# Optimization experiments

Measured on AMD Instinct MI355X. Metric: run time of the kernel, lower is better.

Reference implementation:

```python
import jax, jax.numpy as jnp
import numpy as np

N = 100000  # nodes

def gcn_layer(x, W, b, src, dst, norm):
    # x: [N, Fin] -> [N, Fout]; symmetric-normalized aggregation (PyG GCNConv)
    h = x @ W                                   # linear first (no bias yet)
    msg = h[src] * norm[:, None]                # gather + edge-wise scale
    out = jax.ops.segment_sum(msg, dst, num_segments=N)  # scatter-add to targets
    return out + b

def _prep_edges(edge_index):
    # add self loops
    loops = jnp.arange(N, dtype=edge_index.dtype)
    src = jnp.concatenate([edge_index[0], loops])
    dst = jnp.concatenate([edge_index[1], loops])
    # deg computed on target nodes with unit edge weights
    deg = jax.ops.segment_sum(jnp.ones_like(dst, dtype=jnp.float32), dst, num_segments=N)
    dinv = jnp.where(deg > 0, jax.lax.rsqrt(deg), 0.0)
    norm = dinv[src] * dinv[dst]
    return src, dst, norm

def setup_inputs() -> dict:
    key = jax.random.key(0)
    ks = jax.random.split(key, 8)
    F_in, H1, H2, C = 512, 256, 64, 10
    E = 3200000
    x = jax.random.normal(ks[0], (N, F_in), dtype=jnp.float32)
    edge_index = jax.random.randint(ks[1], (2, E), 0, N, dtype=jnp.int64)
    def glorot(k, fan_in, fan_out):
        s = jnp.sqrt(6.0 / (fan_in + fan_out))
        return jax.random.uniform(k, (fan_in, fan_out), jnp.float32, -s, s)
    return {
        "x": x,
        "edge_index": edge_index,
        "W1": glorot(ks[2], F_in, H1), "b1": jnp.zeros((H1,), jnp.float32),
        "W2": glorot(ks[3], H1, H2),   "b2": jnp.zeros((H2,), jnp.float32),
        "W3": glorot(ks[4], H2, C),    "b3": jnp.zeros((C,), jnp.float32),
    }

def reference(x, edge_index, W1, b1, W2, b2, W3, b3):
    src, dst, norm = _prep_edges(edge_index)
    h = jax.nn.relu(gcn_layer(x, W1, b1, src, dst, norm))
    h = jax.nn.relu(gcn_layer(h, W2, b2, src, dst, norm))
    h = gcn_layer(h, W3, b3, src, dst, norm)
    return jax.nn.log_softmax(h, axis=1)
```

## Files before the change

kernel.cpp:

```cpp
#include <hip/hip_runtime.h>
#include <math.h>

#define NNODES 100000
#define NEDGES 3200000
#define NB 391
#define PB 512
#define CHUNK 6250

typedef __attribute__((ext_vector_type(4))) float f32x4;
typedef __attribute__((ext_vector_type(2))) float f32x2;
typedef __attribute__((ext_vector_type(8))) short bf16x8;

__device__ __forceinline__ float bf2f(ushort u) {
    union { unsigned u; float f; } v; v.u = ((unsigned)u) << 16; return v.f;
}
__device__ __forceinline__ ushort f2bf(float f) {
    union { float f; unsigned u; } v; v.f = f;
    unsigned r = v.u + 0x7FFFu + ((v.u >> 16) & 1u);
    return (ushort)(r >> 16);
}

__device__ __forceinline__ unsigned pack_bf2(float f0, float f1) {
    union { float f; unsigned u; } a, b; a.f = f0; b.f = f1;
#if __has_builtin(__builtin_amdgcn_perm)
    return __builtin_amdgcn_perm(b.u, a.u, 0x07060302u);
#else
    return (b.u & 0xFFFF0000u) | (a.u >> 16);
#endif
}

#if __has_builtin(__builtin_amdgcn_cvt_pk_fp8_f32) && __has_builtin(__builtin_amdgcn_cvt_pk_f32_fp8)
#define FP8_HW 1
#else
#define FP8_HW 0
#endif

__device__ __forceinline__ unsigned fp8enc_sw(float f) {
    union { float f; unsigned u; } v; v.f = f;
    unsigned sign = v.u >> 31;
    float a = fabsf(f);
    if (a >= 448.0f) return (sign << 7) | 0x7E;
    if (a < 0.0009765625f) return sign << 7;
    unsigned u = v.u & 0x7FFFFFFFu;
    u += 0x7FFFFu + ((u >> 20) & 1u);
    int e2 = (int)(u >> 23) - 127;
    if (e2 < -6) {
        int m = (int)(a * 512.0f + 0.5f); if (m > 7) m = 7;
        return (sign << 7) | (unsigned)m;
    }
    if (e2 > 8) return (sign << 7) | 0x7E;
    unsigned mant = (u >> 20) & 7u;
    return (sign << 7) | ((unsigned)(e2 + 7) << 3) | mant;
}
__device__ __forceinline__ float fp8dec_sw(unsigned b) {
    unsigned s = b >> 7, e = (b >> 3) & 0xF, m = b & 7;
    float v;
    if (e == 0) v = (float)m * 0.001953125f;
    else { union { unsigned u; float f; } x; x.u = ((e + 120u) << 23) | (m << 20); v = x.f; }
    return s ? -v : v;
}

__device__ __forceinline__ unsigned char f2fp8(float f) {
#if FP8_HW
    return (unsigned char)(__builtin_amdgcn_cvt_pk_fp8_f32(f, 0.f, 0, false) & 0xFF);
#else
    return (unsigned char)fp8enc_sw(f);
#endif
}
__device__ __forceinline__ void fp8x4_acc(unsigned w, float& ax, float& ay, float& az, float& aw) {
#if FP8_HW
    f32x2 lo = __builtin_amdgcn_cvt_pk_f32_fp8((int)w, false);
    f32x2 hi = __builtin_amdgcn_cvt_pk_f32_fp8((int)w, true);
    ax += lo[0]; ay += lo[1]; az += hi[0]; aw += hi[1];
#else
    ax += fp8dec_sw(w & 0xFF); ay += fp8dec_sw((w >> 8) & 0xFF);
    az += fp8dec_sw((w >> 16) & 0xFF); aw += fp8dec_sw(w >> 24);
#endif
}

__global__ void bucket_hist(const int* __restrict__ dst, int e, int* __restrict__ hist) {
    __shared__ int h[NB];
    const int b = blockIdx.x, t = threadIdx.x;
    for (int j = t; j < NB; j += 256) h[j] = 0;
    __syncthreads();
    const int lo = b * CHUNK;
    int hi = lo + CHUNK; if (hi > e) hi = e;
    for (int i = lo + t; i < hi; i += 256)
        atomicAdd(&h[dst[i] >> 8], 1);
    __syncthreads();
    for (int j = t; j < NB; j += 256) hist[b * NB + j] = h[j];
}

__global__ void scan_buckets(int* __restrict__ hist, int* __restrict__ btotal) {
    __shared__ int s[256];
    const int j = blockIdx.x, t = threadIdx.x;
    int v0 = hist[(2 * t) * NB + j];
    int v1 = hist[(2 * t + 1) * NB + j];
    int p = v0 + v1;
    s[t] = p;
    __syncthreads();
    for (int off = 1; off < 256; off <<= 1) {
        int u = (t >= off) ? s[t - off] : 0;
        __syncthreads();
        s[t] += u;
        __syncthreads();
    }
    int excl = s[t] - p;
    hist[(2 * t) * NB + j] = excl;
    hist[(2 * t + 1) * NB + j] = excl + v0;
    if (t == 255) btotal[j] = s[255];
}

__global__ void scan_btotal(const int* __restrict__ btotal, int* __restrict__ bstart, int e) {
    __shared__ int s[512];
    const int t = threadIdx.x;
    int v = (t < NB) ? btotal[t] : 0;
    s[t] = v;
    __syncthreads();
    for (int off = 1; off < 512; off <<= 1) {
        int u = (t >= off) ? s[t - off] : 0;
        __syncthreads();
        s[t] += u;
        __syncthreads();
    }
    if (t < NB) bstart[t] = s[t] - v;
    if (t == 0) bstart[NB] = e;
}

__global__ void bucket_scatter(const int* __restrict__ src, const int* __restrict__ dst, int e,
                               const int* __restrict__ hist, const int* __restrict__ bstart,
                               unsigned* __restrict__ bucketed) {
    __shared__ int off[NB];
    const int b = blockIdx.x, t = threadIdx.x;
    for (int j = t; j < NB; j += 256) off[j] = bstart[j] + hist[b * NB + j];
    __syncthreads();
    const int lo = b * CHUNK;
    int hi = lo + CHUNK; if (hi > e) hi = e;
    for (int i = lo + t; i < hi; i += 256) {
        int d = dst[i];
        int j = d >> 8;
        int p = atomicAdd(&off[j], 1);
        bucketed[p] = (unsigned)src[i] | ((unsigned)(d & 255) << 24);
    }
}

__global__ void bucket_finalize(const unsigned* __restrict__ bucketed, const int* __restrict__ bstart,
                                float* __restrict__ dinv, int* __restrict__ rowptr,
                                int* __restrict__ esrc, int n, int e) {
    __shared__ int h[256];
    __shared__ int s[256];
    __shared__ int rp[256];
    const int j = blockIdx.x, t = threadIdx.x;
    h[t] = 0;
    __syncthreads();
    const int lo = bstart[j], hi = bstart[j + 1];
    for (int i = lo + t; i < hi; i += 256)
        atomicAdd(&h[bucketed[i] >> 24], 1);
    __syncthreads();
    const int c = h[t] + 1;
    s[t] = c;
    __syncthreads();
    for (int off = 1; off < 256; off <<= 1) {
        int u = (t >= off) ? s[t - off] : 0;
        __syncthreads();
        s[t] += u;
        __syncthreads();
    }
    const int excl = s[t] - c;
    const int base = j << 8;
    const int node = base + t;
    const int myrp = bstart[j] + base + excl;
    rp[t] = myrp;
    if (node < n) {
        dinv[node] = rsqrtf((float)c);
        rowptr[node] = myrp;
        esrc[myrp] = node;
    }
    if (j == 0 && t == 0) rowptr[n] = e + n;
    h[t] = 0;
    __syncthreads();
    for (int i = lo + t; i < hi; i += 256) {
        unsigned ed = bucketed[i];
        int l = ed >> 24;
        int off = atomicAdd(&h[l], 1);
        esrc[rp[l] + 1 + off] = (int)(ed & 0xFFFFFFu);
    }
}

__global__ void conv_wt(const float* __restrict__ W, ushort* __restrict__ Wt,
                        int K, int N, int Npad) {
    int idx = blockIdx.x * blockDim.x + threadIdx.x;
    if (idx >= Npad * K) return;
    int n = idx / K, k = idx % K;
    Wt[idx] = (n < N) ? f2bf(W[(size_t)k * N + n]) : (ushort)0;
}

template <int BM, int BN, int BK, int WM, int WN>
__launch_bounds__(WM* WN * 64)
__global__ void gemm_f32a(const float* __restrict__ A, const ushort* __restrict__ Bt,
                          const float* __restrict__ dinv, unsigned char* __restrict__ Cout,
                          int M, int N, int K) {
    constexpr int NT = WM * WN * 64;
    __shared__ __align__(16) float Asf[BM][BK];
    __shared__ __align__(16) ushort Bs[BN][BK];
    const int tid = threadIdx.x;
    const int wid = tid >> 6, lane = tid & 63;
    const int wr = wid / WN, wc = wid % WN;
    constexpr int TM = BM / WM, TN = BN / WN;
    constexpr int FM = TM / 16, FN = TN / 16;
    const int m0 = blockIdx.y * BM, n0 = blockIdx.x * BN;
    const int ln = lane & 15, ks4 = (lane >> 4) * 2;

    f32x4 acc[FM][FN] = {};

    constexpr int CPRA = BK / 4;
    constexpr int ACH = BM * CPRA;
    constexpr int CPRB = BK / 8;
    constexpr int BCH = BN * CPRB;

    for (int k0 = 0; k0 < K; k0 += BK) {
        #pragma unroll
        for (int it = 0; it < ACH / NT; ++it) {
            int c = it * NT + tid;
            int row = c >> 3, chs = c & 7;
            int gch = chs ^ (row & 7);
            int gm = m0 + row; if (gm >= M) gm = M - 1;
            const float* gp = &A[(size_t)gm * K + k0 + gch * 4];
            __builtin_amdgcn_global_load_lds(
                (const __attribute__((address_space(1))) void*)gp,
                (__attribute__((address_space(3))) void*)((char*)&Asf[0][0] + c * 16),
                16, 0, 0);
        }
        #pragma unroll
        for (int it = 0; it < BCH / NT; ++it) {
            int c = it * NT + tid;
            int row = c / CPRB, ch = c % CPRB;
            const ushort* gp = &Bt[(size_t)(n0 + row) * K + k0 + ch * 8];
            __builtin_amdgcn_global_load_lds(
                (const __attribute__((address_space(1))) void*)gp,
                (__attribute__((address_space(3))) void*)((char*)&Bs[0][0] + c * 16),
                16, 0, 0);
        }
        __syncthreads();

        bf16x8 af[FM], bfr[FN];
        #pragma unroll
        for (int mi = 0; mi < FM; ++mi) {
            int r = wr * TM + mi * 16 + ln;
            const char* rowp = (const char*)&Asf[0][0] + r * (BK * 4);
            float4 a0 = *(const float4*)(rowp + ((ks4 ^ (r & 7)) * 16));
            float4 a1 = *(const float4*)(rowp + (((ks4 + 1) ^ (r & 7)) * 16));
            union { unsigned w[4]; bf16x8 v; } u;
            u.w[0] = pack_bf2(a0.x, a0.y);
            u.w[1] = pack_bf2(a0.z, a0.w);
            u.w[2] = pack_bf2(a1.x, a1.y);
            u.w[3] = pack_bf2(a1.z, a1.w);
            af[mi] = u.v;
        }
        const int ks = (lane >> 4) * 8;
        #pragma unroll
        for (int nj = 0; nj < FN; ++nj)
            bfr[nj] = *(const bf16x8*)&Bs[wc * TN + nj * 16 + ln][ks];
        #pragma unroll
        for (int mi = 0; mi < FM; ++mi)
            #pragma unroll
            for (int nj = 0; nj < FN; ++nj)
                acc[mi][nj] = __builtin_amdgcn_mfma_f32_16x16x32_bf16(af[mi], bfr[nj], acc[mi][nj], 0, 0, 0);
        __syncthreads();
    }

    const int rbase = (lane >> 4) * 4;
    #pragma unroll
    for (int mi = 0; mi < FM; ++mi) {
        #pragma unroll
        for (int r = 0; r < 4; ++r) {
            int gm = m0 + wr * TM + mi * 16 + rbase + r;
            if (gm >= M) continue;
            float d = dinv[gm];
            #pragma unroll
            for (int nj = 0; nj < FN; ++nj) {
                int gn = n0 + wc * TN + nj * 16 + ln;
                Cout[(size_t)gm * N + gn] = f2fp8(acc[mi][nj][r] * d);
            }
        }
    }
}

template <int BM, int BN, int BK, int WM, int WN, int OUTK>
__launch_bounds__(WM* WN * 64)
__global__ void gemm_bf16(const ushort* __restrict__ A, const ushort* __restrict__ Bt,
                          const float* __restrict__ dinv, void* __restrict__ Cout,
                          int M, int N, int K) {
    constexpr int NT = WM * WN * 64;
    __shared__ __align__(16) ushort As[BM][BK];
    __shared__ __align__(16) ushort Bs[BN][BK];
    const int tid = threadIdx.x;
    const int wid = tid >> 6, lane = tid & 63;
    const int wr = wid / WN, wc = wid % WN;
    constexpr int TM = BM / WM, TN = BN / WN;
    constexpr int FM = TM / 16, FN = TN / 16;
    const int m0 = blockIdx.y * BM, n0 = blockIdx.x * BN;
    const int ln = lane & 15, ks = (lane >> 4) * 8;

    f32x4 acc[FM][FN] = {};

    constexpr int ACH = BM * BK / 8;
    constexpr int BCH = BN * BK / 8;
    constexpr int CPR = BK / 8;

    for (int k0 = 0; k0 < K; k0 += BK) {
        #pragma unroll
        for (int it = 0; it < (ACH + NT - 1) / NT; ++it) {
            int c = it * NT + tid;
            if ((ACH % NT == 0) || (c < ACH)) {
                int row = c / CPR, ch = c % CPR;
                int gm = m0 + row; if (gm >= M) gm = M - 1;
                const ushort* gp = &A[(size_t)gm * K + k0 + ch * 8];
                __builtin_amdgcn_global_load_lds(
                    (const __attribute__((address_space(1))) void*)gp,
                    (__attribute__((address_space(3))) void*)((char*)&As[0][0] + c * 16),
                    16, 0, 0);
            }
        }
        #pragma unroll
        for (int it = 0; it < (BCH + NT - 1) / NT; ++it) {
            int c = it * NT + tid;
            if ((BCH % NT == 0) || (c < BCH)) {
                int row = c / CPR, ch = c % CPR;
                const ushort* gp = &Bt[(size_t)(n0 + row) * K + k0 + ch * 8];
                __builtin_amdgcn_global_load_lds(
                    (const __attribute__((address_space(1))) void*)gp,
                    (__attribute__((address_space(3))) void*)((char*)&Bs[0][0] + c * 16),
                    16, 0, 0);
            }
        }
        __syncthreads();

        bf16x8 af[FM], bfr[FN];
        #pragma unroll
        for (int mi = 0; mi < FM; ++mi)
            af[mi] = *(const bf16x8*)&As[wr * TM + mi * 16 + ln][ks];
        #pragma unroll
        for (int nj = 0; nj < FN; ++nj)
            bfr[nj] = *(const bf16x8*)&Bs[wc * TN + nj * 16 + ln][ks];
        #pragma unroll
        for (int mi = 0; mi < FM; ++mi)
            #pragma unroll
            for (int nj = 0; nj < FN; ++nj)
                acc[mi][nj] = __builtin_amdgcn_mfma_f32_16x16x32_bf16(af[mi], bfr[nj], acc[mi][nj], 0, 0, 0);
        __syncthreads();
    }

    const int rbase = (lane >> 4) * 4;
    #pragma unroll
    for (int mi = 0; mi < FM; ++mi) {
        #pragma unroll
        for (int r = 0; r < 4; ++r) {
            int gm = m0 + wr * TM + mi * 16 + rbase + r;
            if (gm >= M) continue;
            float d = dinv[gm];
            #pragma unroll
            for (int nj = 0; nj < FN; ++nj) {
                int gn = n0 + wc * TN + nj * 16 + ln;
                float v = acc[mi][nj][r] * d;
                if (OUTK == 1)      ((float*)Cout)[(size_t)gm * N + gn] = v;
                else if (OUTK == 0) ((ushort*)Cout)[(size_t)gm * N + gn] = f2bf(v);
                else                ((unsigned char*)Cout)[(size_t)gm * N + gn] = f2fp8(v);
            }
        }
    }
}

__global__ void agg1_fp8(const unsigned* __restrict__ h, const int* __restrict__ rowptr,
                         const int* __restrict__ esrc, const float* __restrict__ dinv,
                         const float* __restrict__ bias, ushort* __restrict__ out, int n) {
    const int wid = threadIdx.x >> 6, lane = threadIdx.x & 63;
    const int i = blockIdx.x * 4 + wid;
    if (i >= n) return;
    const int lo = rowptr[i], hi = rowptr[i + 1];
    float ax = 0.f, ay = 0.f, az = 0.f, aw = 0.f;
    int e = lo;
    for (; e + 7 < hi; e += 8) {
        int s[8];
        unsigned w[8];
        #pragma unroll
        for (int q = 0; q < 8; ++q) s[q] = esrc[e + q];
        #pragma unroll
        for (int q = 0; q < 8; ++q) w[q] = h[(size_t)s[q] * 64 + lane];
        #pragma unroll
        for (int q = 0; q < 8; ++q) fp8x4_acc(w[q], ax, ay, az, aw);
    }
    for (; e < hi; ++e)
        fp8x4_acc(h[(size_t)esrc[e] * 64 + lane], ax, ay, az, aw);

    float d = dinv[i];
    const int f0 = lane * 4;
    float4 b = *(const float4*)&bias[f0];
    ushort4 o;
    o.x = f2bf(fmaxf(ax * d + b.x, 0.f));
    o.y = f2bf(fmaxf(ay * d + b.y, 0.f));
    o.z = f2bf(fmaxf(az * d + b.z, 0.f));
    o.w = f2bf(fmaxf(aw * d + b.w, 0.f));
    *(ushort4*)&out[(size_t)i * 256 + f0] = o;
}

__global__ void agg2_fp8(const unsigned* __restrict__ h, const int* __restrict__ rowptr,
                         const int* __restrict__ esrc, const float* __restrict__ dinv,
                         const float* __restrict__ bias, ushort* __restrict__ out, int n) {
    const int g = threadIdx.x >> 4, j = threadIdx.x & 15;
    const int i = blockIdx.x * 16 + g;
    if (i >= n) return;
    const int lo = rowptr[i], hi = rowptr[i + 1];
    float ax = 0.f, ay = 0.f, az = 0.f, aw = 0.f;
    int e = lo;
    for (; e + 3 < hi; e += 4) {
        int s0 = esrc[e], s1 = esrc[e + 1], s2 = esrc[e + 2], s3 = esrc[e + 3];
        unsigned w0 = h[(size_t)s0 * 16 + j];
        unsigned w1 = h[(size_t)s1 * 16 + j];
        unsigned w2 = h[(size_t)s2 * 16 + j];
        unsigned w3 = h[(size_t)s3 * 16 + j];
        fp8x4_acc(w0, ax, ay, az, aw);
        fp8x4_acc(w1, ax, ay, az, aw);
        fp8x4_acc(w2, ax, ay, az, aw);
        fp8x4_acc(w3, ax, ay, az, aw);
    }
    for (; e < hi; ++e)
        fp8x4_acc(h[(size_t)esrc[e] * 16 + j], ax, ay, az, aw);

    float d = dinv[i];
    const int f0 = j * 4;
    float4 b = *(const float4*)&bias[f0];
    ushort4 o;
    o.x = f2bf(fmaxf(ax * d + b.x, 0.f));
    o.y = f2bf(fmaxf(ay * d + b.y, 0.f));
    o.z = f2bf(fmaxf(az * d + b.z, 0.f));
    o.w = f2bf(fmaxf(aw * d + b.w, 0.f));
    *(ushort4*)&out[(size_t)i * 64 + f0] = o;
}

__global__ void agg3_logsoftmax(const ushort* __restrict__ h3, const int* __restrict__ rowptr,
                                const int* __restrict__ esrc, const float* __restrict__ dinv,
                                const float* __restrict__ bias, float* __restrict__ out, int n) {
    const int g = threadIdx.x >> 3, j = threadIdx.x & 7;
    const int i = blockIdx.x * 32 + g;
    if (i >= n) return;
    const int lo = rowptr[i], hi = rowptr[i + 1];
    float a0 = 0.f, a1 = 0.f;
    int e = lo;
    for (; e + 3 < hi; e += 4) {
        int s0 = esrc[e], s1 = esrc[e + 1], s2 = esrc[e + 2], s3 = esrc[e + 3];
        unsigned w0 = *(const unsigned*)&h3[(size_t)s0 * 16 + 2 * j];
        unsigned w1 = *(const unsigned*)&h3[(size_t)s1 * 16 + 2 * j];
        unsigned w2 = *(const unsigned*)&h3[(size_t)s2 * 16 + 2 * j];
        unsigned w3 = *(const unsigned*)&h3[(size_t)s3 * 16 + 2 * j];
        a0 += bf2f((ushort)(w0 & 0xFFFF)) + bf2f((ushort)(w1 & 0xFFFF))
            + bf2f((ushort)(w2 & 0xFFFF)) + bf2f((ushort)(w3 & 0xFFFF));
        a1 += bf2f((ushort)(w0 >> 16)) + bf2f((ushort)(w1 >> 16))
            + bf2f((ushort)(w2 >> 16)) + bf2f((ushort)(w3 >> 16));
    }
    for (; e < hi; ++e) {
        unsigned w = *(const unsigned*)&h3[(size_t)esrc[e] * 16 + 2 * j];
        a0 += bf2f((ushort)(w & 0xFFFF));
        a1 += bf2f((ushort)(w >> 16));
    }
    const int f0 = 2 * j;
    float d = dinv[i];
    float v0 = (f0 < 10) ? (a0 * d + bias[f0]) : -INFINITY;
    float v1 = (f0 + 1 < 10) ? (a1 * d + bias[f0 + 1]) : -INFINITY;
    float m = fmaxf(v0, v1);
    #pragma unroll
    for (int off = 1; off < 8; off <<= 1) m = fmaxf(m, __shfl_xor(m, off, 8));
    float ex = ((f0 < 10) ? expf(v0 - m) : 0.f) + ((f0 + 1 < 10) ? expf(v1 - m) : 0.f);
    #pragma unroll
    for (int off = 1; off < 8; off <<= 1) ex += __shfl_xor(ex, off, 8);
    float ls = logf(ex);
    if (f0 < 10)     out[(size_t)i * 10 + f0] = v0 - m - ls;
    if (f0 + 1 < 10) out[(size_t)i * 10 + f0 + 1] = v1 - m - ls;
}

extern "C" void kernel_launch(void* const* d_in, const int* in_sizes, int n_in,
                              void* d_out, int out_size, void* d_ws, size_t ws_size,
                              hipStream_t stream) {
    const int N = NNODES, E = NEDGES;
    const float* x  = (const float*)d_in[0];
    const int*   ei = (const int*)d_in[1];
    const float* W1 = (const float*)d_in[2];
    const float* b1 = (const float*)d_in[3];
    const float* W2 = (const float*)d_in[4];
    const float* b2 = (const float*)d_in[5];
    const float* W3 = (const float*)d_in[6];
    const float* b3 = (const float*)d_in[7];
    float* out = (float*)d_out;
    const int* src = ei;
    const int* dst = ei + E;

    char* ws = (char*)d_ws;
    size_t off = 0;
    auto alloc = [&](size_t bytes) -> void* {
        void* p = ws + off;
        off = (off + bytes + 255) & ~(size_t)255;
        return p;
    };
    float* dinv   = (float*)alloc((size_t)N * 4);
    int*   rowptr = (int*)alloc((size_t)(N + 1) * 4);
    int*   btotal = (int*)alloc((size_t)NB * 4);
    int*   bstart = (int*)alloc((size_t)(NB + 1) * 4);
    int*   esrc   = (int*)alloc((size_t)(E + N) * 4);
    ushort* W1t   = (ushort*)alloc((size_t)256 * 512 * 2);
    ushort* W2t   = (ushort*)alloc((size_t)64 * 256 * 2);
    ushort* W3t   = (ushort*)alloc((size_t)16 * 64 * 2);
    ushort* h3b   = (ushort*)alloc((size_t)N * 16 * 2);
    ushort* buf1  = (ushort*)alloc((size_t)N * 256 * 2);
    ushort* buf2  = (ushort*)alloc((size_t)N * 256 * 2);
    int*   hist   = (int*)buf1;
    unsigned* bucketed = (unsigned*)buf2;
    unsigned char* h1fp8 = (unsigned char*)buf1;
    unsigned char* h2fp8 = (unsigned char*)buf1;

    const int T = 256;
    bucket_hist<<<PB, T, 0, stream>>>(dst, E, hist);
    scan_buckets<<<NB, T, 0, stream>>>(hist, btotal);
    scan_btotal<<<1, 512, 0, stream>>>(btotal, bstart, E);
    bucket_scatter<<<PB, T, 0, stream>>>(src, dst, E, hist, bstart, bucketed);
    bucket_finalize<<<NB, T, 0, stream>>>(bucketed, bstart, dinv, rowptr, esrc, N, E);

    conv_wt<<<(256 * 512 + T - 1) / T, T, 0, stream>>>(W1, W1t, 512, 256, 256);
    conv_wt<<<(64 * 256 + T - 1) / T, T, 0, stream>>>(W2, W2t, 256, 64, 64);
    conv_wt<<<(16 * 64 + T - 1) / T, T, 0, stream>>>(W3, W3t, 64, 10, 16);

    const int MB = (N + 127) / 128;

    gemm_f32a<128, 256, 32, 2, 4><<<dim3(1, MB), 512, 0, stream>>>(x, W1t, dinv, h1fp8, N, 256, 512);
    agg1_fp8<<<(N + 3) / 4, 256, 0, stream>>>((const unsigned*)h1fp8, rowptr, esrc, dinv, b1, buf2, N);

    gemm_bf16<128, 64, 32, 2, 2, 2><<<dim3(1, MB), 256, 0, stream>>>(buf2, W2t, dinv, h2fp8, N, 64, 256);
    agg2_fp8<<<(N + 15) / 16, 256, 0, stream>>>((const unsigned*)h2fp8, rowptr, esrc, dinv, b2, buf2, N);

    gemm_bf16<128, 16, 32, 4, 1, 0><<<dim3(1, MB), 256, 0, stream>>>(buf2, W3t, dinv, h3b, N, 16, 64);
    agg3_logsoftmax<<<(N + 31) / 32, 256, 0, stream>>>(h3b, rowptr, esrc, dinv, b3, out, N);
}
```

Baseline: 390.4 us.

## Store layer-1/2 activations and W2/W3 in FP8, use FP8 MFMA GEMMs

The aggregation kernels now write their ReLU outputs as FP8 bytes instead of bf16. The second and third GEMMs read those FP8 activations together with FP8-converted weights through the fp8 MFMA instruction. This halves the bytes written by agg1/agg2 and read by the small GEMMs. Accumulators also use packed f32x2 adds after the fp8 conversion. The trade-off is extra quantization error on activations and weights.

```diff
diff --git a/kernel.cpp b/kernel.cpp
--- a/kernel.cpp
+++ b/kernel.cpp
@@ -67,14 +67,13 @@
     return (unsigned char)fp8enc_sw(f);
 #endif
 }
-__device__ __forceinline__ void fp8x4_acc(unsigned w, float& ax, float& ay, float& az, float& aw) {
+__device__ __forceinline__ void fp8x4_acc2(unsigned w, f32x2& a01, f32x2& a23) {
 #if FP8_HW
-    f32x2 lo = __builtin_amdgcn_cvt_pk_f32_fp8((int)w, false);
-    f32x2 hi = __builtin_amdgcn_cvt_pk_f32_fp8((int)w, true);
-    ax += lo[0]; ay += lo[1]; az += hi[0]; aw += hi[1];
+    a01 += __builtin_amdgcn_cvt_pk_f32_fp8((int)w, false);
+    a23 += __builtin_amdgcn_cvt_pk_f32_fp8((int)w, true);
 #else
-    ax += fp8dec_sw(w & 0xFF); ay += fp8dec_sw((w >> 8) & 0xFF);
-    az += fp8dec_sw((w >> 16) & 0xFF); aw += fp8dec_sw(w >> 24);
+    a01[0] += fp8dec_sw(w & 0xFF); a01[1] += fp8dec_sw((w >> 8) & 0xFF);
+    a23[0] += fp8dec_sw((w >> 16) & 0xFF); a23[1] += fp8dec_sw(w >> 24);
 #endif
 }
 
@@ -193,6 +192,14 @@
     if (idx >= Npad * K) return;
     int n = idx / K, k = idx % K;
     Wt[idx] = (n < N) ? f2bf(W[(size_t)k * N + n]) : (ushort)0;
+}
+
+__global__ void conv_wt8(const float* __restrict__ W, unsigned char* __restrict__ Wt,
+                         int K, int N, int Npad) {
+    int idx = blockIdx.x * blockDim.x + threadIdx.x;
+    if (idx >= Npad * K) return;
+    int n = idx / K, k = idx % K;
+    Wt[idx] = (n < N) ? f2fp8(W[(size_t)k * N + n]) : (unsigned char)0;
 }
 
 template <int BM, int BN, int BK, int WM, int WN>
@@ -288,25 +295,25 @@
 
 template <int BM, int BN, int BK, int WM, int WN, int OUTK>
 __launch_bounds__(WM* WN * 64)
-__global__ void gemm_bf16(const ushort* __restrict__ A, const ushort* __restrict__ Bt,
-                          const float* __restrict__ dinv, void* __restrict__ Cout,
-                          int M, int N, int K) {
+__global__ void gemm_fp8(const unsigned char* __restrict__ A, const unsigned char* __restrict__ Bt,
+                         const float* __restrict__ dinv, void* __restrict__ Cout,
+                         int M, int N, int K) {
     constexpr int NT = WM * WN * 64;
-    __shared__ __align__(16) ushort As[BM][BK];
-    __shared__ __align__(16) ushort Bs[BN][BK];
+    __shared__ __align__(16) unsigned char As[BM][BK];
+    __shared__ __align__(16) unsigned char Bs[BN][BK];
     const int tid = threadIdx.x;
     const int wid = tid >> 6, lane = tid & 63;
     const int wr = wid / WN, wc = wid % WN;
     constexpr int TM = BM / WM, TN = BN / WN;
     constexpr int FM = TM / 16, FN = TN / 16;
     const int m0 = blockIdx.y * BM, n0 = blockIdx.x * BN;
-    const int ln = lane & 15, ks = (lane >> 4) * 8;
+    const int ln = lane & 15;
 
     f32x4 acc[FM][FN] = {};
 
-    constexpr int ACH = BM * BK / 8;
-    constexpr int BCH = BN * BK / 8;
-    constexpr int CPR = BK / 8;
+    constexpr int CPR = BK / 16;
+    constexpr int ACH = BM * CPR;
+    constexpr int BCH = BN * CPR;
 
     for (int k0 = 0; k0 < K; k0 += BK) {
         #pragma unroll
@@ -315,7 +322,7 @@
             if ((ACH % NT == 0) || (c < ACH)) {
                 int row = c / CPR, ch = c % CPR;
                 int gm = m0 + row; if (gm >= M) gm = M - 1;
-                const ushort* gp = &A[(size_t)gm * K + k0 + ch * 8];
+                const unsigned char* gp = &A[(size_t)gm * K + k0 + ch * 16];
                 __builtin_amdgcn_global_load_lds(
                     (const __attribute__((address_space(1))) void*)gp,
                     (__attribute__((address_space(3))) void*)((char*)&As[0][0] + c * 16),
@@ -327,7 +334,7 @@
             int c = it * NT + tid;
             if ((BCH % NT == 0) || (c < BCH)) {
                 int row = c / CPR, ch = c % CPR;
-                const ushort* gp = &Bt[(size_t)(n0 + row) * K + k0 + ch * 8];
+                const unsigned char* gp = &Bt[(size_t)(n0 + row) * K + k0 + ch * 16];
                 __builtin_amdgcn_global_load_lds(
                     (const __attribute__((address_space(1))) void*)gp,
                     (__attribute__((address_space(3))) void*)((char*)&Bs[0][0] + c * 16),
@@ -336,18 +343,18 @@
         }
         __syncthreads();
 
-        bf16x8 af[FM], bfr[FN];
+        long af[FM], bfr[FN];
         #pragma unroll
         for (int mi = 0; mi < FM; ++mi)
-            af[mi] = *(const bf16x8*)&As[wr * TM + mi * 16 + ln][ks];
+            af[mi] = ((const long*)&As[0][0])[(wr * TM + mi * 16 + ln) * (BK / 8) + (lane >> 4)];
         #pragma unroll
         for (int nj = 0; nj < FN; ++nj)
-            bfr[nj] = *(const bf16x8*)&Bs[wc * TN + nj * 16 + ln][ks];
+            bfr[nj] = ((const long*)&Bs[0][0])[(wc * TN + nj * 16 + ln) * (BK / 8) + (lane >> 4)];
         #pragma unroll
         for (int mi = 0; mi < FM; ++mi)
             #pragma unroll
             for (int nj = 0; nj < FN; ++nj)
-                acc[mi][nj] = __builtin_amdgcn_mfma_f32_16x16x32_bf16(af[mi], bfr[nj], acc[mi][nj], 0, 0, 0);
+                acc[mi][nj] = __builtin_amdgcn_mfma_f32_16x16x32_fp8_fp8(af[mi], bfr[nj], acc[mi][nj], 0, 0, 0);
         __syncthreads();
     }
 
@@ -363,9 +370,8 @@
             for (int nj = 0; nj < FN; ++nj) {
                 int gn = n0 + wc * TN + nj * 16 + ln;
                 float v = acc[mi][nj][r] * d;
-                if (OUTK == 1)      ((float*)Cout)[(size_t)gm * N + gn] = v;
-                else if (OUTK == 0) ((ushort*)Cout)[(size_t)gm * N + gn] = f2bf(v);
-                else                ((unsigned char*)Cout)[(size_t)gm * N + gn] = f2fp8(v);
+                if (OUTK == 0) ((ushort*)Cout)[(size_t)gm * N + gn] = f2bf(v);
+                else           ((unsigned char*)Cout)[(size_t)gm * N + gn] = f2fp8(v);
             }
         }
     }
@@ -373,12 +379,12 @@
 
 __global__ void agg1_fp8(const unsigned* __restrict__ h, const int* __restrict__ rowptr,
                          const int* __restrict__ esrc, const float* __restrict__ dinv,
-                         const float* __restrict__ bias, ushort* __restrict__ out, int n) {
+                         const float* __restrict__ bias, unsigned char* __restrict__ out, int n) {
     const int wid = threadIdx.x >> 6, lane = threadIdx.x & 63;
     const int i = blockIdx.x * 4 + wid;
     if (i >= n) return;
     const int lo = rowptr[i], hi = rowptr[i + 1];
-    float ax = 0.f, ay = 0.f, az = 0.f, aw = 0.f;
+    f32x2 a01 = {0.f, 0.f}, a23 = {0.f, 0.f};
     int e = lo;
     for (; e + 7 < hi; e += 8) {
         int s[8];
@@ -388,30 +394,30 @@
         #pragma unroll
         for (int q = 0; q < 8; ++q) w[q] = h[(size_t)s[q] * 64 + lane];
         #pragma unroll
-        for (int q = 0; q < 8; ++q) fp8x4_acc(w[q], ax, ay, az, aw);
+        for (int q = 0; q < 8; ++q) fp8x4_acc2(w[q], a01, a23);
     }
     for (; e < hi; ++e)
-        fp8x4_acc(h[(size_t)esrc[e] * 64 + lane], ax, ay, az, aw);
+        fp8x4_acc2(h[(size_t)esrc[e] * 64 + lane], a01, a23);
 
     float d = dinv[i];
     const int f0 = lane * 4;
     float4 b = *(const float4*)&bias[f0];
-    ushort4 o;
-    o.x = f2bf(fmaxf(ax * d + b.x, 0.f));
-    o.y = f2bf(fmaxf(ay * d + b.y, 0.f));
-    o.z = f2bf(fmaxf(az * d + b.z, 0.f));
-    o.w = f2bf(fmaxf(aw * d + b.w, 0.f));
-    *(ushort4*)&out[(size_t)i * 256 + f0] = o;
+    uchar4 o;
+    o.x = f2fp8(fmaxf(a01[0] * d + b.x, 0.f));
+    o.y = f2fp8(fmaxf(a01[1] * d + b.y, 0.f));
+    o.z = f2fp8(fmaxf(a23[0] * d + b.z, 0.f));
+    o.w = f2fp8(fmaxf(a23[1] * d + b.w, 0.f));
+    *(uchar4*)&out[(size_t)i * 256 + f0] = o;
 }
 
 __global__ void agg2_fp8(const unsigned* __restrict__ h, const int* __restrict__ rowptr,
                          const int* __restrict__ esrc, const float* __restrict__ dinv,
-                         const float* __restrict__ bias, ushort* __restrict__ out, int n) {
+                         const float* __restrict__ bias, unsigned char* __restrict__ out, int n) {
     const int g = threadIdx.x >> 4, j = threadIdx.x & 15;
     const int i = blockIdx.x * 16 + g;
     if (i >= n) return;
     const int lo = rowptr[i], hi = rowptr[i + 1];
-    float ax = 0.f, ay = 0.f, az = 0.f, aw = 0.f;
+    f32x2 a01 = {0.f, 0.f}, a23 = {0.f, 0.f};
     int e = lo;
     for (; e + 3 < hi; e += 4) {
         int s0 = esrc[e], s1 = esrc[e + 1], s2 = esrc[e + 2], s3 = esrc[e + 3];
@@ -419,23 +425,23 @@
         unsigned w1 = h[(size_t)s1 * 16 + j];
         unsigned w2 = h[(size_t)s2 * 16 + j];
         unsigned w3 = h[(size_t)s3 * 16 + j];
-        fp8x4_acc(w0, ax, ay, az, aw);
-        fp8x4_acc(w1, ax, ay, az, aw);
-        fp8x4_acc(w2, ax, ay, az, aw);
-        fp8x4_acc(w3, ax, ay, az, aw);
+        fp8x4_acc2(w0, a01, a23);
+        fp8x4_acc2(w1, a01, a23);
+        fp8x4_acc2(w2, a01, a23);
+        fp8x4_acc2(w3, a01, a23);
     }
     for (; e < hi; ++e)
-        fp8x4_acc(h[(size_t)esrc[e] * 16 + j], ax, ay, az, aw);
+        fp8x4_acc2(h[(size_t)esrc[e] * 16 + j], a01, a23);
 
     float d = dinv[i];
     const int f0 = j * 4;
     float4 b = *(const float4*)&bias[f0];
-    ushort4 o;
-    o.x = f2bf(fmaxf(ax * d + b.x, 0.f));
-    o.y = f2bf(fmaxf(ay * d + b.y, 0.f));
-    o.z = f2bf(fmaxf(az * d + b.z, 0.f));
-    o.w = f2bf(fmaxf(aw * d + b.w, 0.f));
-    *(ushort4*)&out[(size_t)i * 64 + f0] = o;
+    uchar4 o;
+    o.x = f2fp8(fmaxf(a01[0] * d + b.x, 0.f));
+    o.y = f2fp8(fmaxf(a01[1] * d + b.y, 0.f));
+    o.z = f2fp8(fmaxf(a23[0] * d + b.z, 0.f));
+    o.w = f2fp8(fmaxf(a23[1] * d + b.w, 0.f));
+    *(uchar4*)&out[(size_t)i * 64 + f0] = o;
 }
 
 __global__ void agg3_logsoftmax(const ushort* __restrict__ h3, const int* __restrict__ rowptr,
@@ -507,15 +513,17 @@
     int*   bstart = (int*)alloc((size_t)(NB + 1) * 4);
     int*   esrc   = (int*)alloc((size_t)(E + N) * 4);
     ushort* W1t   = (ushort*)alloc((size_t)256 * 512 * 2);
-    ushort* W2t   = (ushort*)alloc((size_t)64 * 256 * 2);
-    ushort* W3t   = (ushort*)alloc((size_t)16 * 64 * 2);
+    unsigned char* W2t8 = (unsigned char*)alloc((size_t)64 * 256);
+    unsigned char* W3t8 = (unsigned char*)alloc((size_t)16 * 64);
     ushort* h3b   = (ushort*)alloc((size_t)N * 16 * 2);
     ushort* buf1  = (ushort*)alloc((size_t)N * 256 * 2);
     ushort* buf2  = (ushort*)alloc((size_t)N * 256 * 2);
     int*   hist   = (int*)buf1;
     unsigned* bucketed = (unsigned*)buf2;
     unsigned char* h1fp8 = (unsigned char*)buf1;
+    unsigned char* a1fp8 = (unsigned char*)buf2;
     unsigned char* h2fp8 = (unsigned char*)buf1;
+    unsigned char* a2fp8 = (unsigned char*)buf2;
 
     const int T = 256;
     bucket_hist<<<PB, T, 0, stream>>>(dst, E, hist);
@@ -525,17 +533,17 @@
     bucket_finalize<<<NB, T, 0, stream>>>(bucketed, bstart, dinv, rowptr, esrc, N, E);
 
     conv_wt<<<(256 * 512 + T - 1) / T, T, 0, stream>>>(W1, W1t, 512, 256, 256);
-    conv_wt<<<(64 * 256 + T - 1) / T, T, 0, stream>>>(W2, W2t, 256, 64, 64);
-    conv_wt<<<(16 * 64 + T - 1) / T, T, 0, stream>>>(W3, W3t, 64, 10, 16);
+    conv_wt8<<<(64 * 256 + T - 1) / T, T, 0, stream>>>(W2, W2t8, 256, 64, 64);
+    conv_wt8<<<(16 * 64 + T - 1) / T, T, 0, stream>>>(W3, W3t8, 64, 10, 16);
 
     const int MB = (N + 127) / 128;
 
     gemm_f32a<128, 256, 32, 2, 4><<<dim3(1, MB), 512, 0, stream>>>(x, W1t, dinv, h1fp8, N, 256, 512);
-    agg1_fp8<<<(N + 3) / 4, 256, 0, stream>>>((const unsigned*)h1fp8, rowptr, esrc, dinv, b1, buf2, N);
-
-    gemm_bf16<128, 64, 32, 2, 2, 2><<<dim3(1, MB), 256, 0, stream>>>(buf2, W2t, dinv, h2fp8, N, 64, 256);
-    agg2_fp8<<<(N + 15) / 16, 256, 0, stream>>>((const unsigned*)h2fp8, rowptr, esrc, dinv, b2, buf2, N);
-
-    gemm_bf16<128, 16, 32, 4, 1, 0><<<dim3(1, MB), 256, 0, stream>>>(buf2, W3t, dinv, h3b, N, 16, 64);
+    agg1_fp8<<<(N + 3) / 4, 256, 0, stream>>>((const unsigned*)h1fp8, rowptr, esrc, dinv, b1, a1fp8, N);
+
+    gemm_fp8<128, 64, 32, 2, 2, 2><<<dim3(1, MB), 256, 0, stream>>>(a1fp8, W2t8, dinv, h2fp8, N, 64, 256);
+    agg2_fp8<<<(N + 15) / 16, 256, 0, stream>>>((const unsigned*)h2fp8, rowptr, esrc, dinv, b2, a2fp8, N);
+
+    gemm_fp8<128, 16, 32, 4, 1, 0><<<dim3(1, MB), 256, 0, stream>>>(a2fp8, W3t8, dinv, h3b, N, 16, 64);
     agg3_logsoftmax<<<(N + 31) / 32, 256, 0, stream>>>(h3b, rowptr, esrc, dinv, b3, out, N);
 }
```

Result: faster. 382.5 us (-2.0%).
